# Optimization experiments

Measured on AMD Instinct MI355X. Metric: run time of the kernel, lower is better.

Reference implementation:

```python
import jax, jax.numpy as jnp
import numpy as np

N = 100000   # amino-acid nodes
D = 128      # prot_hidden_dim == input_dim (output_dim)
E = 600000   # edges per relation
L = 3        # prot_num_layers
EPS = 1e-5   # BatchNorm eps


def setup_inputs() -> dict:
    key = jax.random.key(0)
    ks = jax.random.split(key, 16)
    x = jax.random.normal(ks[0], (N, D), jnp.float32)
    seq_src = jax.random.randint(ks[1], (E,), 0, N)
    seq_dst = jax.random.randint(ks[2], (E,), 0, N)
    knn_src = jax.random.randint(ks[3], (E,), 0, N)
    knn_dst = jax.random.randint(ks[4], (E,), 0, N)
    dis_src = jax.random.randint(ks[5], (E,), 0, N)
    dis_dst = jax.random.randint(ks[6], (E,), 0, N)
    # GraphConv weights/biases: [layer, relation, ...]
    Wrel = jax.random.normal(ks[7], (L, 3, D, D), jnp.float32) * (1.0 / np.sqrt(D))
    brel = jax.random.normal(ks[8], (L, 3, D), jnp.float32) * 0.02
    # per-layer fc (last maps hidden -> output_dim == D)
    Wfc = jax.random.normal(ks[9], (L, D, D), jnp.float32) * (1.0 / np.sqrt(D))
    bfc = jax.random.normal(ks[10], (L, D), jnp.float32) * 0.02
    # BatchNorm (eval mode) for layers l=0,1
    gamma = 1.0 + 0.1 * jax.random.normal(ks[11], (L - 1, D), jnp.float32)
    beta = 0.1 * jax.random.normal(ks[12], (L - 1, D), jnp.float32)
    run_mean = 0.1 * jax.random.normal(ks[13], (L - 1, D), jnp.float32)
    run_var = jax.random.uniform(ks[14], (L - 1, D), jnp.float32, 0.5, 1.5)
    return dict(x=x, seq_src=seq_src, seq_dst=seq_dst, knn_src=knn_src,
                knn_dst=knn_dst, dis_src=dis_src, dis_dst=dis_dst,
                Wrel=Wrel, brel=brel, Wfc=Wfc, bfc=bfc,
                gamma=gamma, beta=beta, run_mean=run_mean, run_var=run_var)


def _deg_norms(src, dst):
    # DGL norm='both': out-degree of src, in-degree of dst, clamped to >=1
    ones = jnp.ones(src.shape, jnp.float32)
    out_deg = jnp.clip(jax.ops.segment_sum(ones, src, num_segments=N), 1.0)
    in_deg = jnp.clip(jax.ops.segment_sum(ones, dst, num_segments=N), 1.0)
    return out_deg ** -0.5, in_deg ** -0.5


def reference(x, seq_src, seq_dst, knn_src, knn_dst, dis_src, dis_dst,
              Wrel, brel, Wfc, bfc, gamma, beta, run_mean, run_var):
    rels = [(seq_src, seq_dst), (knn_src, knn_dst), (dis_src, dis_dst)]
    norms = [_deg_norms(s, d) for s, d in rels]
    h = x
    for l in range(L):
        agg = jnp.zeros((N, D), h.dtype)
        for r, (s, d) in enumerate(rels):
            ns, nd = norms[r]
            # GraphConv norm='both', in==out feats: weight first, then propagate
            m = (h @ Wrel[l, r]) * ns[:, None]           # [N, D]
            msg = jax.ops.segment_sum(m[s], d, num_segments=N)  # gather-scatter
            agg = agg + msg * nd[:, None] + brel[l, r]
        h = agg @ Wfc[l] + bfc[l]
        if l < L - 1:
            # eval-mode BatchNorm1d + ReLU (dropout is identity in eval)
            h = (h - run_mean[l]) * jax.lax.rsqrt(run_var[l] + EPS) * gamma[l] + beta[l]
            h = jax.nn.relu(h)
    return h
```

## Files before the change

kernel.cpp:

```cpp
#include <hip/hip_runtime.h>
#include <math.h>

#define N_NODES 100000
#define D 128
#define E_EDGES 600000
#define BN_EPS 1e-5f

typedef __attribute__((ext_vector_type(8))) __bf16 bf16x8;
typedef __attribute__((ext_vector_type(4))) __bf16 bf16x4;
typedef __attribute__((ext_vector_type(16))) float f32x16;

__device__ __forceinline__ int qswz(int row, int q) {
    return (q & 8) | ((q ^ row) & 7);
}
__device__ __forceinline__ int swz(int row, int c) { return c ^ ((row >> 1) & 3); }

__global__ __launch_bounds__(256) void hist_kernel(
    const int* __restrict__ s0, const int* __restrict__ d0,
    const int* __restrict__ s1, const int* __restrict__ d1,
    const int* __restrict__ s2, const int* __restrict__ d2,
    int* __restrict__ outdeg, int* __restrict__ indeg)
{
    const int r = blockIdx.y;
    const int* src = (r == 0) ? s0 : ((r == 1) ? s1 : s2);
    const int* dst = (r == 0) ? d0 : ((r == 1) ? d1 : d2);
    int* od = outdeg + (size_t)r * N_NODES;
    int* id = indeg + (size_t)r * N_NODES;
    int i4 = blockIdx.x * 256 + threadIdx.x;
    if (i4 < E_EDGES / 4) {
        int4 s = ((const int4*)src)[i4];
        int4 d = ((const int4*)dst)[i4];
        atomicAdd(&od[s.x], 1); atomicAdd(&od[s.y], 1);
        atomicAdd(&od[s.z], 1); atomicAdd(&od[s.w], 1);
        atomicAdd(&id[d.x], 1); atomicAdd(&id[d.y], 1);
        atomicAdd(&id[d.z], 1); atomicAdd(&id[d.w], 1);
    }
}

__global__ __launch_bounds__(256) void norm_kernel(
    const int* __restrict__ outdeg, const int* __restrict__ indeg,
    float* __restrict__ ns, float* __restrict__ nd)
{
    int n = blockIdx.x * 256 + threadIdx.x;
    int r = blockIdx.y;
    if (n < N_NODES) {
        int od = outdeg[r * N_NODES + n];
        int id = indeg[r * N_NODES + n];
        ns[r * N_NODES + n] = rsqrtf((float)(od < 1 ? 1 : od));
        nd[r * N_NODES + n] = rsqrtf((float)(id < 1 ? 1 : id));
    }
}

__global__ __launch_bounds__(1024) void scan_kernel(
    const int* __restrict__ indeg, int* __restrict__ rowptr, int* __restrict__ cursor)
{
    const int r = blockIdx.x;
    const int4* deg4 = (const int4*)(indeg + (size_t)r * N_NODES);
    int* rp = rowptr + (size_t)r * (N_NODES + 1);
    int* cur = cursor + (size_t)r * N_NODES;

    __shared__ int wsum[16];
    __shared__ int woff[16];
    __shared__ int chunk_total;

    const int tid = threadIdx.x;
    const int lane = tid & 63;
    const int wid = tid >> 6;
    const int N4 = N_NODES / 4;

    int running = 0;
    for (int base4 = 0; base4 < N4; base4 += 1024) {
        int i4 = base4 + tid;
        int4 v = (i4 < N4) ? deg4[i4] : make_int4(0, 0, 0, 0);
        int s0 = v.x, s1 = s0 + v.y, s2 = s1 + v.z, s3 = s2 + v.w;

        int x = s3;
        #pragma unroll
        for (int off = 1; off < 64; off <<= 1) {
            int y = __shfl_up(x, off);
            if (lane >= off) x += y;
        }
        if (lane == 63) wsum[wid] = x;
        __syncthreads();
        if (wid == 0) {
            int t = (lane < 16) ? wsum[lane] : 0;
            int xx = t;
            #pragma unroll
            for (int off = 1; off < 16; off <<= 1) {
                int y = __shfl_up(xx, off);
                if (lane >= off) xx += y;
            }
            if (lane < 16) woff[lane] = xx - t;
            if (lane == 15) chunk_total = xx;
        }
        __syncthreads();

        int texcl = x - s3;
        int offset = running + woff[wid] + texcl;
        if (i4 < N4) {
            int idx = i4 * 4;
            rp[idx]     = offset;       cur[idx]     = offset;
            rp[idx + 1] = offset + s0;  cur[idx + 1] = offset + s0;
            rp[idx + 2] = offset + s1;  cur[idx + 2] = offset + s1;
            rp[idx + 3] = offset + s2;  cur[idx + 3] = offset + s2;
        }
        running += chunk_total;
    }
    if (tid == 0) rp[N_NODES] = running;
}

__global__ __launch_bounds__(256) void fill_kernel(
    const int* __restrict__ s0, const int* __restrict__ d0,
    const int* __restrict__ s1, const int* __restrict__ d1,
    const int* __restrict__ s2, const int* __restrict__ d2,
    const float* __restrict__ nsv,
    int* __restrict__ cursor, int2* __restrict__ eint)
{
    const int r = blockIdx.y;
    const int* src = (r == 0) ? s0 : ((r == 1) ? s1 : s2);
    const int* dst = (r == 0) ? d0 : ((r == 1) ? d1 : d2);
    int* cur = cursor + (size_t)r * N_NODES;
    int2* eg = eint + (size_t)r * E_EDGES;
    const float* ns_ = nsv + (size_t)r * N_NODES;
    int i = blockIdx.x * 256 + threadIdx.x;
    if (i < E_EDGES) {
        int s = src[i];
        int d = dst[i];
        int pos = atomicAdd(&cur[d], 1);
        eg[pos] = make_int2(s, __float_as_int(ns_[s]));
    }
}

__global__ __launch_bounds__(256) void wprep_kernel(
    const float* __restrict__ Wrel, const float* __restrict__ Wfc,
    const float* __restrict__ gma, const float* __restrict__ rvar,
    __bf16* __restrict__ Whi, __bf16* __restrict__ Wlo)
{
    __shared__ float W1[128][132];
    __shared__ float W2[128][132];
    const int b = blockIdx.x;
    const int l = b / 3;
    const int t = threadIdx.x;

    const float* src1 = Wrel + (size_t)b * D * D;
    const float* src2 = Wfc + (size_t)l * D * D;
    #pragma unroll
    for (int p = 0; p < 16; ++p) {
        int u = t + p * 256;
        int r = u >> 5, f = u & 31;
        float4 v1 = *(const float4*)(src1 + r * D + f * 4);
        float4 v2 = *(const float4*)(src2 + r * D + f * 4);
        *(float4*)&W1[r][f * 4] = v1;
        *(float4*)&W2[r][f * 4] = v2;
    }
    __syncthreads();

    const int row = t >> 1;
    const int cb = (t & 1) * 64;
    float4 acc4[16];
    #pragma unroll
    for (int j = 0; j < 16; ++j) acc4[j] = make_float4(0.f, 0.f, 0.f, 0.f);
    for (int k = 0; k < 128; ++k) {
        float a = W1[row][k];
        #pragma unroll
        for (int j = 0; j < 16; ++j) {
            float4 w = *(const float4*)&W2[k][cb + j * 4];
            acc4[j].x = fmaf(a, w.x, acc4[j].x);
            acc4[j].y = fmaf(a, w.y, acc4[j].y);
            acc4[j].z = fmaf(a, w.z, acc4[j].z);
            acc4[j].w = fmaf(a, w.w, acc4[j].w);
        }
    }
    for (int j = 0; j < 64; ++j) {
        int colj = cb + j;
        float s = 1.0f;
        if (l < 2) s = gma[l * D + colj] * rsqrtf(rvar[l * D + colj] + BN_EPS);
        float v = (&acc4[j >> 2].x)[j & 3] * s;
        __bf16 h = (__bf16)v;
        __bf16 lo = (__bf16)(v - (float)h);
        Whi[((size_t)b * D + colj) * D + row] = h;
        Wlo[((size_t)b * D + colj) * D + row] = lo;
    }
}

__global__ __launch_bounds__(128) void bias_prep_kernel(
    const float* __restrict__ brel, const float* __restrict__ Wfc,
    const float* __restrict__ bfc,
    const float* __restrict__ gma, const float* __restrict__ bta,
    const float* __restrict__ rmean, const float* __restrict__ rvar,
    float* __restrict__ bvec)
{
    int j = threadIdx.x;
    int l = blockIdx.x;
    float acc = bfc[l * D + j];
    for (int k = 0; k < D; ++k) {
        float bs = brel[(l * 3 + 0) * D + k] + brel[(l * 3 + 1) * D + k] + brel[(l * 3 + 2) * D + k];
        acc = fmaf(bs, Wfc[((size_t)l * D + k) * D + j], acc);
    }
    if (l < 2) {
        float s = gma[l * D + j] * rsqrtf(rvar[l * D + j] + BN_EPS);
        acc = acc * s + (bta[l * D + j] - rmean[l * D + j] * s);
    }
    bvec[l * D + j] = acc;
}

__global__ __launch_bounds__(512, 6) void fused_layer_kernel(
    const float* __restrict__ h,
    const int* __restrict__ rowptr,
    const int2* __restrict__ eint,
    const float* __restrict__ ndv,
    const __bf16* __restrict__ Whi,
    const __bf16* __restrict__ Wlo,
    float* __restrict__ out, const float* __restrict__ bias, int relu)
{
    __shared__ __bf16 Ah[64 * 128];
    __shared__ __bf16 Al[64 * 128];
    __shared__ __bf16 Bh[128 * 32];
    __shared__ __bf16 Bl[128 * 32];

    const int t = threadIdx.x;
    const int lane = t & 63;
    const int wid = t >> 6;
    const int wrow = wid & 1;
    const int wcol = wid >> 1;
    const int row0 = blockIdx.x * 64;

    const int g = t >> 3;
    const int gl = t & 7;

    f32x16 acc;
    #pragma unroll
    for (int i = 0; i < 16; ++i) acc[i] = 0.0f;

    for (int r = 0; r < 3; ++r) {
        const int* rp = rowptr + (size_t)r * (N_NODES + 1);
        const int2* eg = eint + (size_t)r * E_EDGES;
        const float* nd_ = ndv + (size_t)r * N_NODES;

        {
            int rowl = g;
            int grow = row0 + rowl;
            float4 a0 = {0,0,0,0}, a1 = {0,0,0,0}, a2 = {0,0,0,0}, a3 = {0,0,0,0};
            if (grow < N_NODES) {
                int beg = rp[grow], end = rp[grow + 1];
                float sc = nd_[grow];
                int e = beg;
                for (; e + 1 < end; e += 2) {
                    int2 e0 = eg[e];
                    int2 e1 = eg[e + 1];
                    float w0 = __int_as_float(e0.y);
                    float w1 = __int_as_float(e1.y);
                    const float* hp0 = h + (size_t)e0.x * D + gl * 4;
                    const float* hp1 = h + (size_t)e1.x * D + gl * 4;
                    float4 u0 = *(const float4*)(hp0);
                    float4 u1 = *(const float4*)(hp0 + 32);
                    float4 u2 = *(const float4*)(hp0 + 64);
                    float4 u3 = *(const float4*)(hp0 + 96);
                    float4 v0 = *(const float4*)(hp1);
                    float4 v1 = *(const float4*)(hp1 + 32);
                    float4 v2 = *(const float4*)(hp1 + 64);
                    float4 v3 = *(const float4*)(hp1 + 96);
                    a0.x = fmaf(w0, u0.x, a0.x); a0.y = fmaf(w0, u0.y, a0.y);
                    a0.z = fmaf(w0, u0.z, a0.z); a0.w = fmaf(w0, u0.w, a0.w);
                    a1.x = fmaf(w0, u1.x, a1.x); a1.y = fmaf(w0, u1.y, a1.y);
                    a1.z = fmaf(w0, u1.z, a1.z); a1.w = fmaf(w0, u1.w, a1.w);
                    a2.x = fmaf(w0, u2.x, a2.x); a2.y = fmaf(w0, u2.y, a2.y);
                    a2.z = fmaf(w0, u2.z, a2.z); a2.w = fmaf(w0, u2.w, a2.w);
                    a3.x = fmaf(w0, u3.x, a3.x); a3.y = fmaf(w0, u3.y, a3.y);
                    a3.z = fmaf(w0, u3.z, a3.z); a3.w = fmaf(w0, u3.w, a3.w);
                    a0.x = fmaf(w1, v0.x, a0.x); a0.y = fmaf(w1, v0.y, a0.y);
                    a0.z = fmaf(w1, v0.z, a0.z); a0.w = fmaf(w1, v0.w, a0.w);
                    a1.x = fmaf(w1, v1.x, a1.x); a1.y = fmaf(w1, v1.y, a1.y);
                    a1.z = fmaf(w1, v1.z, a1.z); a1.w = fmaf(w1, v1.w, a1.w);
                    a2.x = fmaf(w1, v2.x, a2.x); a2.y = fmaf(w1, v2.y, a2.y);
                    a2.z = fmaf(w1, v2.z, a2.z); a2.w = fmaf(w1, v2.w, a2.w);
                    a3.x = fmaf(w1, v3.x, a3.x); a3.y = fmaf(w1, v3.y, a3.y);
                    a3.z = fmaf(w1, v3.z, a3.z); a3.w = fmaf(w1, v3.w, a3.w);
                }
                if (e < end) {
                    int2 e0 = eg[e];
                    float w0 = __int_as_float(e0.y);
                    const float* hp0 = h + (size_t)e0.x * D + gl * 4;
                    float4 u0 = *(const float4*)(hp0);
                    float4 u1 = *(const float4*)(hp0 + 32);
                    float4 u2 = *(const float4*)(hp0 + 64);
                    float4 u3 = *(const float4*)(hp0 + 96);
                    a0.x = fmaf(w0, u0.x, a0.x); a0.y = fmaf(w0, u0.y, a0.y);
                    a0.z = fmaf(w0, u0.z, a0.z); a0.w = fmaf(w0, u0.w, a0.w);
                    a1.x = fmaf(w0, u1.x, a1.x); a1.y = fmaf(w0, u1.y, a1.y);
                    a1.z = fmaf(w0, u1.z, a1.z); a1.w = fmaf(w0, u1.w, a1.w);
                    a2.x = fmaf(w0, u2.x, a2.x); a2.y = fmaf(w0, u2.y, a2.y);
                    a2.z = fmaf(w0, u2.z, a2.z); a2.w = fmaf(w0, u2.w, a2.w);
                    a3.x = fmaf(w0, u3.x, a3.x); a3.y = fmaf(w0, u3.y, a3.y);
                    a3.z = fmaf(w0, u3.z, a3.z); a3.w = fmaf(w0, u3.w, a3.w);
                }
                a0.x *= sc; a0.y *= sc; a0.z *= sc; a0.w *= sc;
                a1.x *= sc; a1.y *= sc; a1.z *= sc; a1.w *= sc;
                a2.x *= sc; a2.y *= sc; a2.z *= sc; a2.w *= sc;
                a3.x *= sc; a3.y *= sc; a3.z *= sc; a3.w *= sc;
            }
            float4 av[4] = {a0, a1, a2, a3};
            #pragma unroll
            for (int j = 0; j < 4; ++j) {
                int q = (gl >> 1) + 4 * j;
                int idx = rowl * 128 + qswz(rowl, q) * 8 + (gl & 1) * 4;
                bf16x4 hv, lv;
                float* ap = &av[j].x;
                #pragma unroll
                for (int c = 0; c < 4; ++c) {
                    __bf16 hb = (__bf16)ap[c];
                    hv[c] = hb;
                    lv[c] = (__bf16)(ap[c] - (float)hb);
                }
                *(bf16x4*)&Ah[idx] = hv;
                *(bf16x4*)&Al[idx] = lv;
            }
        }

        for (int ks = 0; ks < 4; ++ks) {
            {
                int colj = t >> 2;
                int c = t & 3;
                int idx = colj * 32 + swz(colj, c) * 8;
                const __bf16* sh = Whi + (size_t)r * D * D + (size_t)colj * D + ks * 32 + c * 8;
                const __bf16* sl = Wlo + (size_t)r * D * D + (size_t)colj * D + ks * 32 + c * 8;
                *(bf16x8*)&Bh[idx] = *(const bf16x8*)sh;
                *(bf16x8*)&Bl[idx] = *(const bf16x8*)sl;
            }
            __syncthreads();

            const int arow = lane & 31;
            const int kgrp = lane >> 5;
            #pragma unroll
            for (int ksub = 0; ksub < 2; ++ksub) {
                int ac = ksub * 2 + kgrp;
                int arow_g = wrow * 32 + arow;
                int q = ks * 4 + ac;
                int aidx = arow_g * 128 + qswz(arow_g, q) * 8;
                bf16x8 ahv = *(const bf16x8*)&Ah[aidx];
                bf16x8 alv = *(const bf16x8*)&Al[aidx];
                int colg = wcol * 32 + arow;
                int bidx = colg * 32 + swz(colg, ac) * 8;
                bf16x8 bhv = *(const bf16x8*)&Bh[bidx];
                bf16x8 blv = *(const bf16x8*)&Bl[bidx];
                acc = __builtin_amdgcn_mfma_f32_32x32x16_bf16(ahv, bhv, acc, 0, 0, 0);
                acc = __builtin_amdgcn_mfma_f32_32x32x16_bf16(ahv, blv, acc, 0, 0, 0);
                acc = __builtin_amdgcn_mfma_f32_32x32x16_bf16(alv, bhv, acc, 0, 0, 0);
            }
            __syncthreads();
        }
    }

    const int colb = lane & 31;
    const int rq = lane >> 5;
    {
        int colg = wcol * 32 + colb;
        float bv = bias[colg];
        #pragma unroll
        for (int reg = 0; reg < 16; ++reg) {
            int rowl = wrow * 32 + (reg & 3) + 8 * (reg >> 2) + 4 * rq;
            int grow = row0 + rowl;
            if (grow < N_NODES) {
                float z = acc[reg] + bv;
                if (relu) z = z > 0.f ? z : 0.f;
                out[(size_t)grow * D + colg] = z;
            }
        }
    }
}

extern "C" void kernel_launch(void* const* d_in, const int* in_sizes, int n_in,
                              void* d_out, int out_size, void* d_ws, size_t ws_size,
                              hipStream_t stream)
{
    const float* x      = (const float*)d_in[0];
    const int* seq_src  = (const int*)d_in[1];
    const int* seq_dst  = (const int*)d_in[2];
    const int* knn_src  = (const int*)d_in[3];
    const int* knn_dst  = (const int*)d_in[4];
    const int* dis_src  = (const int*)d_in[5];
    const int* dis_dst  = (const int*)d_in[6];
    const float* Wrel   = (const float*)d_in[7];
    const float* brel   = (const float*)d_in[8];
    const float* Wfc    = (const float*)d_in[9];
    const float* bfc    = (const float*)d_in[10];
    const float* gma    = (const float*)d_in[11];
    const float* bta    = (const float*)d_in[12];
    const float* rmean  = (const float*)d_in[13];
    const float* rvar   = (const float*)d_in[14];
    float* out = (float*)d_out;

    const size_t ND = (size_t)N_NODES * D;
    float* ws   = (float*)d_ws;
    float* h0   = ws;
    float* h1   = h0 + ND;
    float* ns_  = h1 + ND;
    float* nd_  = ns_ + 3 * N_NODES;
    float* bvec = nd_ + 3 * N_NODES;
    __bf16* Whi = (__bf16*)(bvec + 3 * D);
    __bf16* Wlo = Whi + (size_t)9 * D * D;
    int* outdeg = (int*)(Wlo + (size_t)9 * D * D);
    int* indeg  = outdeg + 3 * N_NODES;
    int* rowptr = indeg + 3 * N_NODES;
    int* cursor = rowptr + 3 * (N_NODES + 1) + 1;
    int2* eint  = (int2*)(cursor + 3 * N_NODES);

    hipMemsetAsync(outdeg, 0, (size_t)6 * N_NODES * sizeof(int), stream);
    hist_kernel<<<dim3((E_EDGES / 4 + 255) / 256, 3), 256, 0, stream>>>(
        seq_src, seq_dst, knn_src, knn_dst, dis_src, dis_dst, outdeg, indeg);
    norm_kernel<<<dim3((N_NODES + 255) / 256, 3), 256, 0, stream>>>(outdeg, indeg, ns_, nd_);
    scan_kernel<<<3, 1024, 0, stream>>>(indeg, rowptr, cursor);
    fill_kernel<<<dim3((E_EDGES + 255) / 256, 3), 256, 0, stream>>>(
        seq_src, seq_dst, knn_src, knn_dst, dis_src, dis_dst, ns_, cursor, eint);

    wprep_kernel<<<9, 256, 0, stream>>>(Wrel, Wfc, gma, rvar, Whi, Wlo);
    bias_prep_kernel<<<3, 128, 0, stream>>>(brel, Wfc, bfc, gma, bta, rmean, rvar, bvec);

    const int GB = (N_NODES + 63) / 64;
    fused_layer_kernel<<<GB, 512, 0, stream>>>(
        x, rowptr, eint, nd_, Whi, Wlo, h0, bvec, 1);
    fused_layer_kernel<<<GB, 512, 0, stream>>>(
        h0, rowptr, eint, nd_, Whi + (size_t)3 * D * D, Wlo + (size_t)3 * D * D,
        h1, bvec + D, 1);
    fused_layer_kernel<<<GB, 512, 0, stream>>>(
        h1, rowptr, eint, nd_, Whi + (size_t)6 * D * D, Wlo + (size_t)6 * D * D,
        out, bvec + 2 * D, 0);
}
```

Measured before the change: 946.0 us.

## Remap gather threads to 16 per row with 4-edge unroll and pad B LDS

The neighbor gather now uses 16 threads per node row, each loading 8 contiguous floats, and every thread handles two rows. The edge loop is unrolled by four so more independent row loads are in flight. The A tile swizzle is changed so each thread can store one bf16x8 per row, and the B tile row stride is padded to 40 to reduce LDS bank conflicts. The cost is more registers and a longer per-thread serial gather over two rows.

```diff
diff --git a/kernel.cpp b/kernel.cpp
--- a/kernel.cpp
+++ b/kernel.cpp
@@ -10,9 +10,9 @@
 typedef __attribute__((ext_vector_type(4))) __bf16 bf16x4;
 typedef __attribute__((ext_vector_type(16))) float f32x16;
 
-__device__ __forceinline__ int qswz(int row, int q) {
-    return (q & 8) | ((q ^ row) & 7);
-}
+#define BSTRIDE 40
+
+__device__ __forceinline__ int qswz(int row, int q) { return q ^ (row & 15); }
 __device__ __forceinline__ int swz(int row, int c) { return c ^ ((row >> 1) & 3); }
 
 __global__ __launch_bounds__(256) void hist_kernel(
@@ -204,6 +204,12 @@
     bvec[l * D + j] = acc;
 }
 
+#define FMA8(W_, U_, V_)                                                       \
+    acc0.x = fmaf(W_, U_.x, acc0.x); acc0.y = fmaf(W_, U_.y, acc0.y);          \
+    acc0.z = fmaf(W_, U_.z, acc0.z); acc0.w = fmaf(W_, U_.w, acc0.w);          \
+    acc1.x = fmaf(W_, V_.x, acc1.x); acc1.y = fmaf(W_, V_.y, acc1.y);          \
+    acc1.z = fmaf(W_, V_.z, acc1.z); acc1.w = fmaf(W_, V_.w, acc1.w);
+
 __global__ __launch_bounds__(512, 6) void fused_layer_kernel(
     const float* __restrict__ h,
     const int* __restrict__ rowptr,
@@ -215,8 +221,8 @@
 {
     __shared__ __bf16 Ah[64 * 128];
     __shared__ __bf16 Al[64 * 128];
-    __shared__ __bf16 Bh[128 * 32];
-    __shared__ __bf16 Bl[128 * 32];
+    __shared__ __bf16 Bh[128 * BSTRIDE];
+    __shared__ __bf16 Bl[128 * BSTRIDE];
 
     const int t = threadIdx.x;
     const int lane = t & 63;
@@ -224,9 +230,8 @@
     const int wrow = wid & 1;
     const int wcol = wid >> 1;
     const int row0 = blockIdx.x * 64;
-
-    const int g = t >> 3;
-    const int gl = t & 7;
+    const int g = t >> 4;
+    const int gl = t & 15;
 
     f32x16 acc;
     #pragma unroll
@@ -237,91 +242,68 @@
         const int2* eg = eint + (size_t)r * E_EDGES;
         const float* nd_ = ndv + (size_t)r * N_NODES;
 
-        {
-            int rowl = g;
+        #pragma unroll
+        for (int rr = 0; rr < 2; ++rr) {
+            int rowl = g * 2 + rr;
             int grow = row0 + rowl;
-            float4 a0 = {0,0,0,0}, a1 = {0,0,0,0}, a2 = {0,0,0,0}, a3 = {0,0,0,0};
+            float4 acc0 = {0, 0, 0, 0}, acc1 = {0, 0, 0, 0};
             if (grow < N_NODES) {
                 int beg = rp[grow], end = rp[grow + 1];
                 float sc = nd_[grow];
                 int e = beg;
-                for (; e + 1 < end; e += 2) {
-                    int2 e0 = eg[e];
-                    int2 e1 = eg[e + 1];
-                    float w0 = __int_as_float(e0.y);
-                    float w1 = __int_as_float(e1.y);
-                    const float* hp0 = h + (size_t)e0.x * D + gl * 4;
-                    const float* hp1 = h + (size_t)e1.x * D + gl * 4;
-                    float4 u0 = *(const float4*)(hp0);
-                    float4 u1 = *(const float4*)(hp0 + 32);
-                    float4 u2 = *(const float4*)(hp0 + 64);
-                    float4 u3 = *(const float4*)(hp0 + 96);
-                    float4 v0 = *(const float4*)(hp1);
-                    float4 v1 = *(const float4*)(hp1 + 32);
-                    float4 v2 = *(const float4*)(hp1 + 64);
-                    float4 v3 = *(const float4*)(hp1 + 96);
-                    a0.x = fmaf(w0, u0.x, a0.x); a0.y = fmaf(w0, u0.y, a0.y);
-                    a0.z = fmaf(w0, u0.z, a0.z); a0.w = fmaf(w0, u0.w, a0.w);
-                    a1.x = fmaf(w0, u1.x, a1.x); a1.y = fmaf(w0, u1.y, a1.y);
-                    a1.z = fmaf(w0, u1.z, a1.z); a1.w = fmaf(w0, u1.w, a1.w);
-                    a2.x = fmaf(w0, u2.x, a2.x); a2.y = fmaf(w0, u2.y, a2.y);
-                    a2.z = fmaf(w0, u2.z, a2.z); a2.w = fmaf(w0, u2.w, a2.w);
-                    a3.x = fmaf(w0, u3.x, a3.x); a3.y = fmaf(w0, u3.y, a3.y);
-                    a3.z = fmaf(w0, u3.z, a3.z); a3.w = fmaf(w0, u3.w, a3.w);
-                    a0.x = fmaf(w1, v0.x, a0.x); a0.y = fmaf(w1, v0.y, a0.y);
-                    a0.z = fmaf(w1, v0.z, a0.z); a0.w = fmaf(w1, v0.w, a0.w);
-                    a1.x = fmaf(w1, v1.x, a1.x); a1.y = fmaf(w1, v1.y, a1.y);
-                    a1.z = fmaf(w1, v1.z, a1.z); a1.w = fmaf(w1, v1.w, a1.w);
-                    a2.x = fmaf(w1, v2.x, a2.x); a2.y = fmaf(w1, v2.y, a2.y);
-                    a2.z = fmaf(w1, v2.z, a2.z); a2.w = fmaf(w1, v2.w, a2.w);
-                    a3.x = fmaf(w1, v3.x, a3.x); a3.y = fmaf(w1, v3.y, a3.y);
-                    a3.z = fmaf(w1, v3.z, a3.z); a3.w = fmaf(w1, v3.w, a3.w);
+                for (; e + 4 <= end; e += 4) {
+                    int2 r0 = eg[e], r1 = eg[e + 1], r2 = eg[e + 2], r3 = eg[e + 3];
+                    const float* p0 = h + (size_t)r0.x * D + gl * 8;
+                    const float* p1 = h + (size_t)r1.x * D + gl * 8;
+                    const float* p2 = h + (size_t)r2.x * D + gl * 8;
+                    const float* p3 = h + (size_t)r3.x * D + gl * 8;
+                    float4 u0 = *(const float4*)p0, v0 = *(const float4*)(p0 + 4);
+                    float4 u1 = *(const float4*)p1, v1 = *(const float4*)(p1 + 4);
+                    float4 u2 = *(const float4*)p2, v2 = *(const float4*)(p2 + 4);
+                    float4 u3 = *(const float4*)p3, v3 = *(const float4*)(p3 + 4);
+                    float w0 = __int_as_float(r0.y), w1 = __int_as_float(r1.y);
+                    float w2 = __int_as_float(r2.y), w3 = __int_as_float(r3.y);
+                    FMA8(w0, u0, v0); FMA8(w1, u1, v1);
+                    FMA8(w2, u2, v2); FMA8(w3, u3, v3);
+                }
+                if (e + 2 <= end) {
+                    int2 r0 = eg[e], r1 = eg[e + 1];
+                    const float* p0 = h + (size_t)r0.x * D + gl * 8;
+                    const float* p1 = h + (size_t)r1.x * D + gl * 8;
+                    float4 u0 = *(const float4*)p0, v0 = *(const float4*)(p0 + 4);
+                    float4 u1 = *(const float4*)p1, v1 = *(const float4*)(p1 + 4);
+                    float w0 = __int_as_float(r0.y), w1 = __int_as_float(r1.y);
+                    FMA8(w0, u0, v0); FMA8(w1, u1, v1);
+                    e += 2;
                 }
                 if (e < end) {
-                    int2 e0 = eg[e];
-                    float w0 = __int_as_float(e0.y);
-                    const float* hp0 = h + (size_t)e0.x * D + gl * 4;
-                    float4 u0 = *(const float4*)(hp0);
-                    float4 u1 = *(const float4*)(hp0 + 32);
-                    float4 u2 = *(const float4*)(hp0 + 64);
-                    float4 u3 = *(const float4*)(hp0 + 96);
-                    a0.x = fmaf(w0, u0.x, a0.x); a0.y = fmaf(w0, u0.y, a0.y);
-                    a0.z = fmaf(w0, u0.z, a0.z); a0.w = fmaf(w0, u0.w, a0.w);
-                    a1.x = fmaf(w0, u1.x, a1.x); a1.y = fmaf(w0, u1.y, a1.y);
-                    a1.z = fmaf(w0, u1.z, a1.z); a1.w = fmaf(w0, u1.w, a1.w);
-                    a2.x = fmaf(w0, u2.x, a2.x); a2.y = fmaf(w0, u2.y, a2.y);
-                    a2.z = fmaf(w0, u2.z, a2.z); a2.w = fmaf(w0, u2.w, a2.w);
-                    a3.x = fmaf(w0, u3.x, a3.x); a3.y = fmaf(w0, u3.y, a3.y);
-                    a3.z = fmaf(w0, u3.z, a3.z); a3.w = fmaf(w0, u3.w, a3.w);
+                    int2 r0 = eg[e];
+                    const float* p0 = h + (size_t)r0.x * D + gl * 8;
+                    float4 u0 = *(const float4*)p0, v0 = *(const float4*)(p0 + 4);
+                    float w0 = __int_as_float(r0.y);
+                    FMA8(w0, u0, v0);
                 }
-                a0.x *= sc; a0.y *= sc; a0.z *= sc; a0.w *= sc;
-                a1.x *= sc; a1.y *= sc; a1.z *= sc; a1.w *= sc;
-                a2.x *= sc; a2.y *= sc; a2.z *= sc; a2.w *= sc;
-                a3.x *= sc; a3.y *= sc; a3.z *= sc; a3.w *= sc;
-            }
-            float4 av[4] = {a0, a1, a2, a3};
+                acc0.x *= sc; acc0.y *= sc; acc0.z *= sc; acc0.w *= sc;
+                acc1.x *= sc; acc1.y *= sc; acc1.z *= sc; acc1.w *= sc;
+            }
+            float a[8] = {acc0.x, acc0.y, acc0.z, acc0.w, acc1.x, acc1.y, acc1.z, acc1.w};
+            bf16x8 hv, lv;
             #pragma unroll
-            for (int j = 0; j < 4; ++j) {
-                int q = (gl >> 1) + 4 * j;
-                int idx = rowl * 128 + qswz(rowl, q) * 8 + (gl & 1) * 4;
-                bf16x4 hv, lv;
-                float* ap = &av[j].x;
-                #pragma unroll
-                for (int c = 0; c < 4; ++c) {
-                    __bf16 hb = (__bf16)ap[c];
-                    hv[c] = hb;
-                    lv[c] = (__bf16)(ap[c] - (float)hb);
-                }
-                *(bf16x4*)&Ah[idx] = hv;
-                *(bf16x4*)&Al[idx] = lv;
-            }
+            for (int c = 0; c < 8; ++c) {
+                __bf16 hb = (__bf16)a[c];
+                hv[c] = hb;
+                lv[c] = (__bf16)(a[c] - (float)hb);
+            }
+            int idxA = rowl * 128 + qswz(rowl, gl) * 8;
+            *(bf16x8*)&Ah[idxA] = hv;
+            *(bf16x8*)&Al[idxA] = lv;
         }
 
         for (int ks = 0; ks < 4; ++ks) {
             {
                 int colj = t >> 2;
                 int c = t & 3;
-                int idx = colj * 32 + swz(colj, c) * 8;
+                int idx = colj * BSTRIDE + swz(colj, c) * 8;
                 const __bf16* sh = Whi + (size_t)r * D * D + (size_t)colj * D + ks * 32 + c * 8;
                 const __bf16* sl = Wlo + (size_t)r * D * D + (size_t)colj * D + ks * 32 + c * 8;
                 *(bf16x8*)&Bh[idx] = *(const bf16x8*)sh;
@@ -335,12 +317,11 @@
             for (int ksub = 0; ksub < 2; ++ksub) {
                 int ac = ksub * 2 + kgrp;
                 int arow_g = wrow * 32 + arow;
-                int q = ks * 4 + ac;
-                int aidx = arow_g * 128 + qswz(arow_g, q) * 8;
+                int aidx = arow_g * 128 + qswz(arow_g, ks * 4 + ac) * 8;
                 bf16x8 ahv = *(const bf16x8*)&Ah[aidx];
                 bf16x8 alv = *(const bf16x8*)&Al[aidx];
                 int colg = wcol * 32 + arow;
-                int bidx = colg * 32 + swz(colg, ac) * 8;
+                int bidx = colg * BSTRIDE + swz(colg, ac) * 8;
                 bf16x8 bhv = *(const bf16x8*)&Bh[bidx];
                 bf16x8 blv = *(const bf16x8*)&Bl[bidx];
                 acc = __builtin_amdgcn_mfma_f32_32x32x16_bf16(ahv, bhv, acc, 0, 0, 0);
@@ -362,7 +343,7 @@
             int grow = row0 + rowl;
             if (grow < N_NODES) {
                 float z = acc[reg] + bv;
-                if (relu) z = z > 0.f ? z : 0.f;
+                if (relu) z = fmaxf(z, 0.f);
                 out[(size_t)grow * D + colg] = z;
             }
         }
@@ -405,6 +386,10 @@
     int* cursor = rowptr + 3 * (N_NODES + 1) + 1;
     int2* eint  = (int2*)(cursor + 3 * N_NODES);
 
+    const int* srcs[3] = {seq_src, knn_src, dis_src};
+    const int* dsts[3] = {seq_dst, knn_dst, dis_dst};
+    (void)srcs; (void)dsts;
+
     hipMemsetAsync(outdeg, 0, (size_t)6 * N_NODES * sizeof(int), stream);
     hist_kernel<<<dim3((E_EDGES / 4 + 255) / 256, 3), 256, 0, stream>>>(
         seq_src, seq_dst, knn_src, knn_dst, dis_src, dis_dst, outdeg, indeg);
```

Measured after the change: 975.5 us. 3.1% more time.
